# Kernel optimization log

Hardware: AMD Instinct MI355X
Metric: run time of the kernel (lower is better)

Reference implementation:

```python
import jax, jax.numpy as jnp
import numpy as np

B, T, E, H = 2, 2048, 1024, 16
S = E // H
LN_EPS = 1e-5


def _layer_norm(x, w, b):
    # normalize over last axis (head dim s)
    mu = jnp.mean(x, axis=-1, keepdims=True)
    var = jnp.mean(jnp.square(x - mu), axis=-1, keepdims=True)
    return (x - mu) * jax.lax.rsqrt(var + LN_EPS) * w + b


def setup_inputs() -> dict:
    key = jax.random.key(0)
    ks = jax.random.split(key, 7)
    scale = 0.02
    return {
        "queries": jax.random.normal(ks[0], (B, T, E), dtype=jnp.float32),
        "keys": jax.random.normal(ks[1], (B, T, E), dtype=jnp.float32),
        "values": jax.random.normal(ks[2], (B, T, E), dtype=jnp.float32),
        "Wq": jax.random.normal(ks[3], (E, E), dtype=jnp.float32) * scale,
        "Wk": jax.random.normal(ks[4], (E, E), dtype=jnp.float32) * scale,
        "Wv": jax.random.normal(ks[5], (E, E), dtype=jnp.float32) * scale,
        "Wo": jax.random.normal(ks[6], (E, E), dtype=jnp.float32) * scale,
        "bo": jnp.zeros((E,), dtype=jnp.float32),
        "q_ln_w": jnp.ones((S,), dtype=jnp.float32),
        "q_ln_b": jnp.zeros((S,), dtype=jnp.float32),
        "k_ln_w": jnp.ones((S,), dtype=jnp.float32),
        "k_ln_b": jnp.zeros((S,), dtype=jnp.float32),
    }


def reference(queries, keys, values, Wq, Wk, Wv, Wo, bo, q_ln_w, q_ln_b, k_ln_w, k_ln_b):
    b, tq, e = queries.shape
    tk = keys.shape[1]
    h, s = H, S

    q = (queries @ Wq).reshape(b, tq, h, s)
    k = (keys @ Wk).reshape(b, tk, h, s)
    v = (values @ Wv).reshape(b, tk, h, s)

    # kqnorm: per-head LayerNorm over s
    q = _layer_norm(q, q_ln_w, q_ln_b)
    k = _layer_norm(k, k_ln_w, k_ln_b)

    # NOTE: original scales q and k each by emb**(-1/4) (NOT head_dim)
    inv4 = jnp.asarray(e, q.dtype) ** -0.25
    q = q * inv4
    k = k * inv4

    dot = jnp.einsum("bqhs,bkhs->bhqk", q, k)  # [b,h,tq,tk]

    # causal mask (mask_diagonal=False -> keep diagonal): mask j > i
    causal = jnp.tril(jnp.ones((tq, tk), dtype=bool))
    dot = jnp.where(causal, dot, jnp.asarray(-jnp.inf, dot.dtype))

    attn = jax.nn.softmax(dot, axis=-1)

    out = jnp.einsum("bhqk,bkhs->bqhs", attn, v).reshape(b, tq, e)
    return out @ Wo + bo
```

## Files before the change

kernel.cpp:

```cpp
#include <hip/hip_runtime.h>

#define Tdim 2048
#define Edim 1024
#define Hdim 16
#define Sdim 64
#define Mdim 4096
#define LN_EPS 1e-5f
#define QKSCALE 0.21233045007200477f

typedef __bf16 bf16x8 __attribute__((ext_vector_type(8)));
typedef float f32x4 __attribute__((ext_vector_type(4)));

__device__ __forceinline__ unsigned short f2bf(float f) {
  union { float f; unsigned int u; } c; c.f = f;
  unsigned int u = c.u;
  return (unsigned short)((u + 0x7FFFu + ((u >> 16) & 1u)) >> 16);
}

__device__ __forceinline__ float exp2fast(float x) {
  float r;
  asm("v_exp_f32 %0, %1" : "=v"(r) : "v"(x));
  return r;
}

__device__ __forceinline__ void gl_lds16(const void* g, void* l) {
  __builtin_amdgcn_global_load_lds(
      (const __attribute__((address_space(1))) void*)g,
      (__attribute__((address_space(3))) void*)l, 16, 0, 0);
}

__device__ __forceinline__ unsigned int pk2bf(unsigned int lo, unsigned int hi) {
  return __builtin_amdgcn_perm(hi, lo, 0x07060302u);
}

__global__ __launch_bounds__(256) void prep_k(
    const float* __restrict__ X0, const float* __restrict__ X1, const float* __restrict__ X2,
    unsigned short* __restrict__ Y0, unsigned short* __restrict__ Y1,
    unsigned short* __restrict__ Y2,
    const float* __restrict__ W0, const float* __restrict__ W1,
    const float* __restrict__ W2, const float* __restrict__ W3,
    unsigned short* __restrict__ O0, unsigned short* __restrict__ O1,
    unsigned short* __restrict__ O2, unsigned short* __restrict__ O3) {
  int bid = blockIdx.x, tid = threadIdx.x;
  if (bid < 6144) {
    int zi = bid >> 11, blk = bid & 2047;
    const float* X = zi == 0 ? X0 : zi == 1 ? X1 : X2;
    unsigned short* Y = zi == 0 ? Y0 : zi == 1 ? Y1 : Y2;
    size_t i = ((size_t)blk * 256 + tid) * 8;
    uint4 a = *(const uint4*)&X[i];
    uint4 b = *(const uint4*)&X[i + 4];
    uint4 o;
    o.x = pk2bf(a.x, a.y);
    o.y = pk2bf(a.z, a.w);
    o.z = pk2bf(b.x, b.y);
    o.w = pk2bf(b.z, b.w);
    *(uint4*)&Y[i] = o;
  } else {
    int wb = bid - 6144;
    int zi = wb >> 10, tile = wb & 1023;
    const float* W = zi == 0 ? W0 : zi == 1 ? W1 : zi == 2 ? W2 : W3;
    unsigned short* O = zi == 0 ? O0 : zi == 1 ? O1 : zi == 2 ? O2 : O3;
    __shared__ float t[32][33];
    int n0 = (tile & 31) * 32, k0 = (tile >> 5) * 32;
    int tx = tid & 31, ty = tid >> 5;
    for (int yy = ty; yy < 32; yy += 8)
      t[yy][tx] = W[(size_t)(k0 + yy) * Edim + n0 + tx];
    __syncthreads();
    for (int yy = ty; yy < 32; yy += 8)
      O[(size_t)(n0 + yy) * Edim + k0 + tx] = f2bf(t[tx][yy]);
  }
}

__global__ __launch_bounds__(256, 4) void qkv_k(
    const unsigned short* __restrict__ Qa, const unsigned short* __restrict__ Ka,
    const unsigned short* __restrict__ Va,
    const unsigned short* __restrict__ Bq, const unsigned short* __restrict__ Bk,
    const unsigned short* __restrict__ Bv,
    const float* __restrict__ qlnw, const float* __restrict__ qlnb,
    const float* __restrict__ klnw, const float* __restrict__ klnb,
    unsigned short* __restrict__ Oq, unsigned short* __restrict__ Ok,
    unsigned short* __restrict__ Ov) {
  __shared__ unsigned short As[128 * 32];
  __shared__ unsigned short Bs[128 * 32];
  int f = blockIdx.x;
  int L = (f & 7) * 96 + (f >> 3);
  int bx = L & 7, by = (L >> 3) & 31, z = L >> 8;
  const unsigned short* A = z == 0 ? Qa : z == 1 ? Ka : Va;
  const unsigned short* Bt = z == 0 ? Bq : z == 1 ? Bk : Bv;
  const float* lnw = z == 0 ? qlnw : klnw;
  const float* lnb = z == 0 ? qlnb : klnb;
  unsigned short* obf = z == 0 ? Oq : z == 1 ? Ok : Ov;

  int tid = threadIdx.x, lane = tid & 63, w = tid >> 6;
  int wr = w >> 1, wc = w & 1;
  int lg = lane >> 4, l15 = lane & 15;
  int cr = lane >> 2, sl = lane & 3;
  int m0 = by * 128, n0 = bx * 128;

  f32x4 acc[4][4];
#pragma unroll
  for (int i = 0; i < 4; ++i)
#pragma unroll
    for (int j = 0; j < 4; ++j) acc[i][j] = f32x4{0.f, 0.f, 0.f, 0.f};

  for (int ks = 0; ks < 32; ++ks) {
    int k0 = ks * 32;
    __syncthreads();
#pragma unroll
    for (int q = 0; q < 2; ++q) {
      int c = w * 2 + q, r = c * 16 + cr;
      gl_lds16(&A[(size_t)(m0 + r) * Edim + k0 + ((sl ^ (r & 3)) * 8)], &As[c * 512]);
    }
#pragma unroll
    for (int q = 0; q < 2; ++q) {
      int c = w * 2 + q, r = c * 16 + cr;
      gl_lds16(&Bt[(size_t)(n0 + r) * Edim + k0 + ((sl ^ (r & 3)) * 8)], &Bs[c * 512]);
    }
    __syncthreads();
    const unsigned short* pA = (z == 2) ? &Bs[0] : &As[0];
    const unsigned short* pB = (z == 2) ? &As[0] : &Bs[0];
    bf16x8 a[4], bb[4];
#pragma unroll
    for (int i = 0; i < 4; ++i) {
      int r = wr * 64 + i * 16 + l15;
      a[i] = *(const bf16x8*)&pA[r * 32 + ((lg ^ (r & 3)) * 8)];
    }
#pragma unroll
    for (int j = 0; j < 4; ++j) {
      int r = wc * 64 + j * 16 + l15;
      bb[j] = *(const bf16x8*)&pB[r * 32 + ((lg ^ (r & 3)) * 8)];
    }
    __builtin_amdgcn_s_setprio(1);
#pragma unroll
    for (int i = 0; i < 4; ++i)
#pragma unroll
      for (int j = 0; j < 4; ++j)
        acc[i][j] = __builtin_amdgcn_mfma_f32_16x16x32_bf16(a[i], bb[j], acc[i][j], 0, 0, 0);
    __builtin_amdgcn_s_setprio(0);
  }

  if (z < 2) {
    int mb = m0 + wr * 64;
    int h = (n0 >> 6) + wc;
#pragma unroll
    for (int i = 0; i < 4; ++i) {
#pragma unroll
      for (int r = 0; r < 4; ++r) {
        float xv[4];
#pragma unroll
        for (int j = 0; j < 4; ++j) xv[j] = acc[i][j][r];
        float sum = xv[0] + xv[1] + xv[2] + xv[3];
        float sq = xv[0] * xv[0] + xv[1] * xv[1] + xv[2] * xv[2] + xv[3] * xv[3];
#pragma unroll
        for (int off = 1; off < 16; off <<= 1) {
          sum += __shfl_xor(sum, off);
          sq += __shfl_xor(sq, off);
        }
        float mean = sum * (1.f / 64.f);
        float var = sq * (1.f / 64.f) - mean * mean;
        float rstd = rsqrtf(var + LN_EPS);
        int m = mb + i * 16 + (lg << 2) + r;
        int bb2 = m >> 11, tt = m & 2047;
        size_t base = ((size_t)(bb2 * Hdim + h) * Tdim + tt) * Sdim;
#pragma unroll
        for (int j = 0; j < 4; ++j) {
          int s = j * 16 + l15;
          float ov = ((xv[j] - mean) * rstd * lnw[s] + lnb[s]) * QKSCALE;
          obf[base + s] = f2bf(ov);
        }
      }
    }
  } else {
#pragma unroll
    for (int i = 0; i < 4; ++i)
#pragma unroll
      for (int r = 0; r < 4; ++r) {
        int hc = n0 + wr * 64 + i * 16 + (lg << 2) + r;
        int h = hc >> 6, s = hc & 63;
#pragma unroll
        for (int j = 0; j < 4; ++j) {
          int tk = m0 + wc * 64 + j * 16 + l15;
          int bb2 = tk >> 11, tt = tk & 2047;
          obf[(((size_t)(bb2 * Hdim + h) * Sdim + s)) * Tdim + tt] = f2bf(acc[i][j][r]);
        }
      }
  }
}

__global__ __launch_bounds__(256, 4) void gemmo_k(
    const unsigned short* __restrict__ A, const unsigned short* __restrict__ Bt,
    const float* __restrict__ bias, float* __restrict__ ofp) {
  __shared__ unsigned short As[128 * 32];
  __shared__ unsigned short Bs[64 * 32];
  int f = blockIdx.x;
  int L = (f & 7) * 64 + (f >> 3);
  int bx = L & 15, by = L >> 4;
  int tid = threadIdx.x, lane = tid & 63, w = tid >> 6;
  int wr = w >> 1, wc = w & 1;
  int lg = lane >> 4, l15 = lane & 15;
  int cr = lane >> 2, sl = lane & 3;
  int m0 = by * 128, n0 = bx * 64;

  f32x4 acc[4][2];
#pragma unroll
  for (int i = 0; i < 4; ++i)
#pragma unroll
    for (int j = 0; j < 2; ++j) acc[i][j] = f32x4{0.f, 0.f, 0.f, 0.f};

  for (int ks = 0; ks < 32; ++ks) {
    int k0 = ks * 32;
    __syncthreads();
#pragma unroll
    for (int q = 0; q < 2; ++q) {
      int c = w * 2 + q, r = c * 16 + cr;
      gl_lds16(&A[(size_t)(m0 + r) * Edim + k0 + ((sl ^ (r & 3)) * 8)], &As[c * 512]);
    }
    {
      int c = w, r = c * 16 + cr;
      gl_lds16(&Bt[(size_t)(n0 + r) * Edim + k0 + ((sl ^ (r & 3)) * 8)], &Bs[c * 512]);
    }
    __syncthreads();
    bf16x8 a[4], bb[2];
#pragma unroll
    for (int i = 0; i < 4; ++i) {
      int r = wr * 64 + i * 16 + l15;
      a[i] = *(const bf16x8*)&As[r * 32 + ((lg ^ (r & 3)) * 8)];
    }
#pragma unroll
    for (int j = 0; j < 2; ++j) {
      int r = wc * 32 + j * 16 + l15;
      bb[j] = *(const bf16x8*)&Bs[r * 32 + ((lg ^ (r & 3)) * 8)];
    }
    __builtin_amdgcn_s_setprio(1);
#pragma unroll
    for (int i = 0; i < 4; ++i)
#pragma unroll
      for (int j = 0; j < 2; ++j)
        acc[i][j] = __builtin_amdgcn_mfma_f32_16x16x32_bf16(a[i], bb[j], acc[i][j], 0, 0, 0);
    __builtin_amdgcn_s_setprio(0);
  }

  int mb = m0 + wr * 64, nb = n0 + wc * 32;
#pragma unroll
  for (int i = 0; i < 4; ++i)
#pragma unroll
    for (int r = 0; r < 4; ++r) {
      int m = mb + i * 16 + (lg << 2) + r;
#pragma unroll
      for (int j = 0; j < 2; ++j) {
        int n = nb + j * 16 + l15;
        ofp[(size_t)m * Edim + n] = acc[i][j][r] + bias[n];
      }
    }
}

__global__ __launch_bounds__(256) void flash_k(
    const unsigned short* __restrict__ Qn, const unsigned short* __restrict__ Kn,
    const unsigned short* __restrict__ Vb, unsigned short* __restrict__ Ob) {
  __shared__ unsigned short Qs[4096];
  __shared__ unsigned short Ks[2][4096];
  __shared__ unsigned short Vt[2][4096];
  __shared__ unsigned short Ps[4][1024];

  int wid0 = blockIdx.x;
  int idx = wid0 >> 3;
  int bh = (wid0 & 7) * 4 + (idx & 3);
  int qseg = 31 - (idx >> 2);
  int nt = qseg + 1;

  int tid = threadIdx.x, lane = tid & 63, w = tid >> 6;
  int lg = lane >> 4, l15 = lane & 15;
  int lr = lane >> 3, ls = lane & 7;
  const unsigned short* Qg = Qn + ((size_t)bh * Tdim + (size_t)qseg * 64) * Sdim;
  const unsigned short* Kg = Kn + (size_t)bh * Tdim * Sdim;
  const unsigned short* Vg = Vb + (size_t)bh * Sdim * Tdim;
  int b = bh >> 4, h = bh & 15;

  auto stageK = [&](int tt, int kb) {
    const unsigned short* src = Kg + (size_t)tt * 64 * 64;
#pragma unroll
    for (int q = 0; q < 2; ++q) {
      int c = w * 2 + q, r = c * 8 + lr;
      gl_lds16(&src[r * 64 + ((ls ^ (r & 7)) * 8)], &Ks[kb][c * 512]);
    }
  };
  auto stageV = [&](int tt, int vb) {
    const unsigned short* src = Vg + tt * 64;
#pragma unroll
    for (int q = 0; q < 2; ++q) {
      int c = w * 2 + q, r = c * 8 + lr;
      gl_lds16(&src[(size_t)r * Tdim + ((ls ^ (r & 7)) * 8)], &Vt[vb][c * 512]);
    }
  };

#pragma unroll
  for (int q = 0; q < 2; ++q) {
    int c = w * 2 + q, r = c * 8 + lr;
    gl_lds16(&Qg[r * 64 + ((ls ^ (r & 7)) * 8)], &Qs[c * 512]);
  }
  stageK(0, 0);
  stageV(0, 0);

  float mrun = -1e30f;
  float lrun = 0.f;
  f32x4 o[4];
#pragma unroll
  for (int js = 0; js < 4; ++js) o[js] = f32x4{0.f, 0.f, 0.f, 0.f};

  __syncthreads();

  bf16x8 aq[2];
  {
    int rq = w * 16 + l15;
    aq[0] = *(const bf16x8*)&Qs[rq * 64 + ((lg ^ (rq & 7)) * 8)];
    aq[1] = *(const bf16x8*)&Qs[rq * 64 + (((4 + lg) ^ (rq & 7)) * 8)];
  }
  unsigned int swz = (unsigned)(l15 & 7) << 4;

  for (int t = 0; t < nt; ++t) {
    int cur = t & 1;
    if (t + 1 < nt) {
      stageK(t + 1, cur ^ 1);
      stageV(t + 1, cur ^ 1);
    }
    f32x4 sf[4];
#pragma unroll
    for (int j = 0; j < 4; ++j) sf[j] = f32x4{0.f, 0.f, 0.f, 0.f};
    const unsigned short* Kc = &Ks[cur][0];
    __builtin_amdgcn_s_setprio(1);
#pragma unroll
    for (int kx = 0; kx < 2; ++kx) {
#pragma unroll
      for (int j = 0; j < 4; ++j) {
        int rk = j * 16 + l15;
        bf16x8 ak = *(const bf16x8*)&Kc[rk * 64 + (((kx * 4 + lg) ^ (rk & 7)) * 8)];
        sf[j] = __builtin_amdgcn_mfma_f32_16x16x32_bf16(ak, aq[kx], sf[j], 0, 0, 0);
      }
    }
    __builtin_amdgcn_s_setprio(0);
    if (t == qseg) {
#pragma unroll
      for (int j = 0; j < 4; ++j)
#pragma unroll
        for (int rr = 0; rr < 4; ++rr)
          if (j * 16 + (lg << 2) + rr > w * 16 + l15) sf[j][rr] = -1e30f;
    }
    float mx = fmaxf(fmaxf(fmaxf(sf[0][0], sf[0][1]), fmaxf(sf[0][2], sf[0][3])),
                     fmaxf(fmaxf(sf[1][0], sf[1][1]), fmaxf(sf[1][2], sf[1][3])));
    mx = fmaxf(mx, fmaxf(fmaxf(fmaxf(sf[2][0], sf[2][1]), fmaxf(sf[2][2], sf[2][3])),
                         fmaxf(fmaxf(sf[3][0], sf[3][1]), fmaxf(sf[3][2], sf[3][3]))));
    mx = fmaxf(mx, __shfl_xor(mx, 16));
    mx = fmaxf(mx, __shfl_xor(mx, 32));
    if (__any(mx > mrun + 8.f)) {
      float mnew = fmaxf(mrun, mx);
      float alpha = exp2fast(mrun - mnew);
      mrun = mnew;
      lrun *= alpha;
      float ar[4];
#pragma unroll
      for (int rr = 0; rr < 4; ++rr)
        ar[rr] = __shfl(alpha, (lg << 4) | ((lg << 2) + rr));
#pragma unroll
      for (int js = 0; js < 4; ++js)
#pragma unroll
        for (int rr = 0; rr < 4; ++rr) o[js][rr] *= ar[rr];
    }
    unsigned short* Pw = &Ps[w][0];
#pragma unroll
    for (int j = 0; j < 4; ++j) {
      float p0 = exp2fast(sf[j][0] - mrun);
      float p1 = exp2fast(sf[j][1] - mrun);
      float p2 = exp2fast(sf[j][2] - mrun);
      float p3 = exp2fast(sf[j][3] - mrun);
      lrun += (p0 + p1) + (p2 + p3);
      union { float f; unsigned int u; } c0{p0}, c1{p1}, c2{p2}, c3{p3};
      uint2 wv;
      wv.x = pk2bf(c0.u, c1.u);
      wv.y = pk2bf(c2.u, c3.u);
      *(uint2*)((char*)Pw + l15 * 128 + ((j * 32 + lg * 8) ^ swz)) = wv;
    }
    const unsigned short* Vc = &Vt[cur][0];
    __builtin_amdgcn_s_setprio(1);
#pragma unroll
    for (int kx = 0; kx < 2; ++kx) {
      bf16x8 ap = *(const bf16x8*)((char*)Pw + l15 * 128 + ((kx * 64 + lg * 16) ^ swz));
#pragma unroll
      for (int js = 0; js < 4; ++js) {
        int rv = js * 16 + l15;
        bf16x8 bv = *(const bf16x8*)&Vc[rv * 64 + (((kx * 4 + lg) ^ (rv & 7)) * 8)];
        o[js] = __builtin_amdgcn_mfma_f32_16x16x32_bf16(ap, bv, o[js], 0, 0, 0);
      }
    }
    __builtin_amdgcn_s_setprio(0);
    __syncthreads();
  }

  float l = lrun;
  l += __shfl_xor(l, 16);
  l += __shfl_xor(l, 32);
  float inv = 1.f / l;
#pragma unroll
  for (int rr = 0; rr < 4; ++rr) {
    float invr = __shfl(inv, (lg << 4) | ((lg << 2) + rr));
    int tg = qseg * 64 + w * 16 + (lg << 2) + rr;
    size_t base = ((size_t)b * Tdim + tg) * Edim + h * 64;
#pragma unroll
    for (int js = 0; js < 4; ++js) Ob[base + js * 16 + l15] = f2bf(o[js][rr] * invr);
  }
}

extern "C" void kernel_launch(void* const* d_in, const int* in_sizes, int n_in,
                              void* d_out, int out_size, void* d_ws, size_t ws_size,
                              hipStream_t stream) {
  const float* queries = (const float*)d_in[0];
  const float* keys    = (const float*)d_in[1];
  const float* values  = (const float*)d_in[2];
  const float* Wq = (const float*)d_in[3];
  const float* Wk = (const float*)d_in[4];
  const float* Wv = (const float*)d_in[5];
  const float* Wo = (const float*)d_in[6];
  const float* bo = (const float*)d_in[7];
  const float* qlnw = (const float*)d_in[8];
  const float* qlnb = (const float*)d_in[9];
  const float* klnw = (const float*)d_in[10];
  const float* klnb = (const float*)d_in[11];
  float* out = (float*)d_out;

  unsigned short* Wtq = (unsigned short*)d_ws;
  unsigned short* Wtk = Wtq + 1024 * 1024;
  unsigned short* Wtv = Wtk + 1024 * 1024;
  unsigned short* Wto = Wtv + 1024 * 1024;
  unsigned short* Qn  = Wto + 1024 * 1024;
  unsigned short* Kn  = Qn + (size_t)Mdim * Edim;
  unsigned short* Vb  = Kn + (size_t)Mdim * Edim;
  unsigned short* Qa  = Vb + (size_t)Mdim * Edim;
  unsigned short* Ka  = Qa + (size_t)Mdim * Edim;
  unsigned short* Va  = Ka + (size_t)Mdim * Edim;
  unsigned short* Ob  = Qa;

  prep_k<<<10240, 256, 0, stream>>>(queries, keys, values, Qa, Ka, Va,
                                    Wq, Wk, Wv, Wo, Wtq, Wtk, Wtv, Wto);
  qkv_k<<<768, 256, 0, stream>>>(Qa, Ka, Va, Wtq, Wtk, Wtv,
                                 qlnw, qlnb, klnw, klnb, Qn, Kn, Vb);
  flash_k<<<1024, 256, 0, stream>>>(Qn, Kn, Vb, Ob);
  gemmo_k<<<512, 256, 0, stream>>>(Ob, Wto, bo, out);
}
```

Baseline: 213.3 us.

## Transpose MFMA operand roles for vectorized epilogue stores; load Q directly to registers

Swaps the A/B operand roles in the QKV projection and output GEMMs so each lane holds four consecutive output columns, which allows packed 8-byte bf16 stores and float4 fp32 stores instead of scattered scalar stores. The LayerNorm reduction now runs mostly within a lane with only two cross-lane shuffles. The flash kernel drops the Q shared-memory staging and loads Q fragments straight from global memory into registers. Q/K LayerNorm outputs also switch from round-to-nearest to truncating bf16 packing, which slightly changes numerics.

```diff
diff --git a/kernel.cpp b/kernel.cpp
--- a/kernel.cpp
+++ b/kernel.cpp
@@ -31,6 +31,11 @@
 
 __device__ __forceinline__ unsigned int pk2bf(unsigned int lo, unsigned int hi) {
   return __builtin_amdgcn_perm(hi, lo, 0x07060302u);
+}
+
+__device__ __forceinline__ unsigned int pk2bf_f(float lo, float hi) {
+  union { float f; unsigned int u; } a{lo}, b{hi};
+  return pk2bf(a.u, b.u);
 }
 
 __global__ __launch_bounds__(256) void prep_k(
@@ -117,8 +122,8 @@
       gl_lds16(&Bt[(size_t)(n0 + r) * Edim + k0 + ((sl ^ (r & 3)) * 8)], &Bs[c * 512]);
     }
     __syncthreads();
-    const unsigned short* pA = (z == 2) ? &Bs[0] : &As[0];
-    const unsigned short* pB = (z == 2) ? &As[0] : &Bs[0];
+    const unsigned short* pA = (z == 2) ? &As[0] : &Bs[0];
+    const unsigned short* pB = (z == 2) ? &Bs[0] : &As[0];
     bf16x8 a[4], bb[4];
 #pragma unroll
     for (int i = 0; i < 4; ++i) {
@@ -140,50 +145,59 @@
   }
 
   if (z < 2) {
-    int mb = m0 + wr * 64;
+    int h = (n0 >> 6) + wr;
+    float4 lw[4], lb[4];
+#pragma unroll
+    for (int i = 0; i < 4; ++i) {
+      lw[i] = *(const float4*)&lnw[i * 16 + lg * 4];
+      lb[i] = *(const float4*)&lnb[i * 16 + lg * 4];
+    }
+#pragma unroll
+    for (int j = 0; j < 4; ++j) {
+      float sum = 0.f, sq = 0.f;
+#pragma unroll
+      for (int i = 0; i < 4; ++i)
+#pragma unroll
+        for (int rr = 0; rr < 4; ++rr) {
+          float v = acc[i][j][rr];
+          sum += v;
+          sq += v * v;
+        }
+      sum += __shfl_xor(sum, 16); sum += __shfl_xor(sum, 32);
+      sq  += __shfl_xor(sq, 16);  sq  += __shfl_xor(sq, 32);
+      float mean = sum * (1.f / 64.f);
+      float var = sq * (1.f / 64.f) - mean * mean;
+      float rstd = rsqrtf(var + LN_EPS);
+      int m = m0 + wc * 64 + j * 16 + l15;
+      int bb2 = m >> 11, tt = m & 2047;
+      size_t base = ((size_t)(bb2 * Hdim + h) * Tdim + tt) * Sdim;
+#pragma unroll
+      for (int i = 0; i < 4; ++i) {
+        float o0 = ((acc[i][j][0] - mean) * rstd * lw[i].x + lb[i].x) * QKSCALE;
+        float o1 = ((acc[i][j][1] - mean) * rstd * lw[i].y + lb[i].y) * QKSCALE;
+        float o2 = ((acc[i][j][2] - mean) * rstd * lw[i].z + lb[i].z) * QKSCALE;
+        float o3 = ((acc[i][j][3] - mean) * rstd * lw[i].w + lb[i].w) * QKSCALE;
+        uint2 wv;
+        wv.x = pk2bf_f(o0, o1);
+        wv.y = pk2bf_f(o2, o3);
+        *(uint2*)&obf[base + i * 16 + lg * 4] = wv;
+      }
+    }
+  } else {
     int h = (n0 >> 6) + wc;
 #pragma unroll
-    for (int i = 0; i < 4; ++i) {
-#pragma unroll
-      for (int r = 0; r < 4; ++r) {
-        float xv[4];
-#pragma unroll
-        for (int j = 0; j < 4; ++j) xv[j] = acc[i][j][r];
-        float sum = xv[0] + xv[1] + xv[2] + xv[3];
-        float sq = xv[0] * xv[0] + xv[1] * xv[1] + xv[2] * xv[2] + xv[3] * xv[3];
-#pragma unroll
-        for (int off = 1; off < 16; off <<= 1) {
-          sum += __shfl_xor(sum, off);
-          sq += __shfl_xor(sq, off);
-        }
-        float mean = sum * (1.f / 64.f);
-        float var = sq * (1.f / 64.f) - mean * mean;
-        float rstd = rsqrtf(var + LN_EPS);
-        int m = mb + i * 16 + (lg << 2) + r;
+    for (int j = 0; j < 4; ++j) {
+      int s = j * 16 + l15;
+#pragma unroll
+      for (int i = 0; i < 4; ++i) {
+        int m = m0 + wr * 64 + i * 16 + lg * 4;
         int bb2 = m >> 11, tt = m & 2047;
-        size_t base = ((size_t)(bb2 * Hdim + h) * Tdim + tt) * Sdim;
-#pragma unroll
-        for (int j = 0; j < 4; ++j) {
-          int s = j * 16 + l15;
-          float ov = ((xv[j] - mean) * rstd * lnw[s] + lnb[s]) * QKSCALE;
-          obf[base + s] = f2bf(ov);
-        }
+        uint2 wv;
+        wv.x = pk2bf_f(acc[i][j][0], acc[i][j][1]);
+        wv.y = pk2bf_f(acc[i][j][2], acc[i][j][3]);
+        *(uint2*)&obf[((size_t)(bb2 * Hdim + h) * Sdim + s) * Tdim + tt] = wv;
       }
     }
-  } else {
-#pragma unroll
-    for (int i = 0; i < 4; ++i)
-#pragma unroll
-      for (int r = 0; r < 4; ++r) {
-        int hc = n0 + wr * 64 + i * 16 + (lg << 2) + r;
-        int h = hc >> 6, s = hc & 63;
-#pragma unroll
-        for (int j = 0; j < 4; ++j) {
-          int tk = m0 + wc * 64 + j * 16 + l15;
-          int bb2 = tk >> 11, tt = tk & 2047;
-          obf[(((size_t)(bb2 * Hdim + h) * Sdim + s)) * Tdim + tt] = f2bf(acc[i][j][r]);
-        }
-      }
   }
 }
 
@@ -201,11 +215,11 @@
   int cr = lane >> 2, sl = lane & 3;
   int m0 = by * 128, n0 = bx * 64;
 
-  f32x4 acc[4][2];
-#pragma unroll
-  for (int i = 0; i < 4; ++i)
-#pragma unroll
-    for (int j = 0; j < 2; ++j) acc[i][j] = f32x4{0.f, 0.f, 0.f, 0.f};
+  f32x4 acc[2][4];
+#pragma unroll
+  for (int i = 0; i < 2; ++i)
+#pragma unroll
+    for (int j = 0; j < 4; ++j) acc[i][j] = f32x4{0.f, 0.f, 0.f, 0.f};
 
   for (int ks = 0; ks < 32; ++ks) {
     int k0 = ks * 32;
@@ -220,44 +234,48 @@
       gl_lds16(&Bt[(size_t)(n0 + r) * Edim + k0 + ((sl ^ (r & 3)) * 8)], &Bs[c * 512]);
     }
     __syncthreads();
-    bf16x8 a[4], bb[2];
-#pragma unroll
-    for (int i = 0; i < 4; ++i) {
-      int r = wr * 64 + i * 16 + l15;
-      a[i] = *(const bf16x8*)&As[r * 32 + ((lg ^ (r & 3)) * 8)];
-    }
-#pragma unroll
-    for (int j = 0; j < 2; ++j) {
-      int r = wc * 32 + j * 16 + l15;
-      bb[j] = *(const bf16x8*)&Bs[r * 32 + ((lg ^ (r & 3)) * 8)];
+    bf16x8 a[2], bb[4];
+#pragma unroll
+    for (int i = 0; i < 2; ++i) {
+      int r = wr * 32 + i * 16 + l15;
+      a[i] = *(const bf16x8*)&Bs[r * 32 + ((lg ^ (r & 3)) * 8)];
+    }
+#pragma unroll
+    for (int j = 0; j < 4; ++j) {
+      int r = wc * 64 + j * 16 + l15;
+      bb[j] = *(const bf16x8*)&As[r * 32 + ((lg ^ (r & 3)) * 8)];
     }
     __builtin_amdgcn_s_setprio(1);
 #pragma unroll
-    for (int i = 0; i < 4; ++i)
-#pragma unroll
-      for (int j = 0; j < 2; ++j)
+    for (int i = 0; i < 2; ++i)
+#pragma unroll
+      for (int j = 0; j < 4; ++j)
         acc[i][j] = __builtin_amdgcn_mfma_f32_16x16x32_bf16(a[i], bb[j], acc[i][j], 0, 0, 0);
     __builtin_amdgcn_s_setprio(0);
   }
 
-  int mb = m0 + wr * 64, nb = n0 + wc * 32;
-#pragma unroll
-  for (int i = 0; i < 4; ++i)
-#pragma unroll
-    for (int r = 0; r < 4; ++r) {
-      int m = mb + i * 16 + (lg << 2) + r;
-#pragma unroll
-      for (int j = 0; j < 2; ++j) {
-        int n = nb + j * 16 + l15;
-        ofp[(size_t)m * Edim + n] = acc[i][j][r] + bias[n];
-      }
-    }
+  float4 bv[2];
+#pragma unroll
+  for (int i = 0; i < 2; ++i) bv[i] = *(const float4*)&bias[n0 + wr * 32 + i * 16 + lg * 4];
+#pragma unroll
+  for (int j = 0; j < 4; ++j) {
+    int m = m0 + wc * 64 + j * 16 + l15;
+#pragma unroll
+    for (int i = 0; i < 2; ++i) {
+      int nb = n0 + wr * 32 + i * 16 + lg * 4;
+      float4 ov;
+      ov.x = acc[i][j][0] + bv[i].x;
+      ov.y = acc[i][j][1] + bv[i].y;
+      ov.z = acc[i][j][2] + bv[i].z;
+      ov.w = acc[i][j][3] + bv[i].w;
+      *(float4*)&ofp[(size_t)m * Edim + nb] = ov;
+    }
+  }
 }
 
 __global__ __launch_bounds__(256) void flash_k(
     const unsigned short* __restrict__ Qn, const unsigned short* __restrict__ Kn,
     const unsigned short* __restrict__ Vb, unsigned short* __restrict__ Ob) {
-  __shared__ unsigned short Qs[4096];
   __shared__ unsigned short Ks[2][4096];
   __shared__ unsigned short Vt[2][4096];
   __shared__ unsigned short Ps[4][1024];
@@ -293,11 +311,13 @@
     }
   };
 
-#pragma unroll
-  for (int q = 0; q < 2; ++q) {
-    int c = w * 2 + q, r = c * 8 + lr;
-    gl_lds16(&Qg[r * 64 + ((ls ^ (r & 7)) * 8)], &Qs[c * 512]);
-  }
+  bf16x8 aq[2];
+  {
+    const unsigned short* Qrow = Qg + (size_t)(w * 16 + l15) * 64;
+    aq[0] = *(const bf16x8*)&Qrow[lg * 8];
+    aq[1] = *(const bf16x8*)&Qrow[32 + lg * 8];
+  }
+
   stageK(0, 0);
   stageV(0, 0);
 
@@ -309,12 +329,6 @@
 
   __syncthreads();
 
-  bf16x8 aq[2];
-  {
-    int rq = w * 16 + l15;
-    aq[0] = *(const bf16x8*)&Qs[rq * 64 + ((lg ^ (rq & 7)) * 8)];
-    aq[1] = *(const bf16x8*)&Qs[rq * 64 + (((4 + lg) ^ (rq & 7)) * 8)];
-  }
   unsigned int swz = (unsigned)(l15 & 7) << 4;
 
   for (int t = 0; t < nt; ++t) {
@@ -373,10 +387,9 @@
       float p2 = exp2fast(sf[j][2] - mrun);
       float p3 = exp2fast(sf[j][3] - mrun);
       lrun += (p0 + p1) + (p2 + p3);
-      union { float f; unsigned int u; } c0{p0}, c1{p1}, c2{p2}, c3{p3};
       uint2 wv;
-      wv.x = pk2bf(c0.u, c1.u);
-      wv.y = pk2bf(c2.u, c3.u);
+      wv.x = pk2bf_f(p0, p1);
+      wv.y = pk2bf_f(p2, p3);
       *(uint2*)((char*)Pw + l15 * 128 + ((j * 32 + lg * 8) ^ swz)) = wv;
     }
     const unsigned short* Vc = &Vt[cur][0];
```

Result: no change. 216.4 us (+1.5%).
